# Optimization experiments

Measured on AMD Instinct MI355X. Metric: run time of the kernel, lower is better.

Reference implementation:

```python
import jax, jax.numpy as jnp
import numpy as np
from jax import lax

DN = ('NCDHW', 'OIDHW', 'NCDHW')
ALPHA = 0.1
EPS = 1e-5


def conv3d(x, w, b, padding=1):
    out = lax.conv_general_dilated(x, w, (1, 1, 1), [(padding, padding)] * 3,
                                   dimension_numbers=DN)
    return out + b[None, :, None, None, None]


def conv_transpose3d(x, w, b):
    # PyTorch ConvTranspose3d(k=4, s=2, p=1): equivalent to conv with
    # lhs_dilation=2, flipped kernel, padding k-1-p = 2 per side. Output = 2*D.
    w_c = jnp.flip(jnp.transpose(w, (1, 0, 2, 3, 4)), axis=(2, 3, 4))  # [out,in,4,4,4]
    out = lax.conv_general_dilated(x, w_c, (1, 1, 1), [(2, 2)] * 3,
                                   lhs_dilation=(2, 2, 2), dimension_numbers=DN)
    return out + b[None, :, None, None, None]


def instance_norm(x):
    m = jnp.mean(x, axis=(2, 3, 4), keepdims=True)
    v = jnp.var(x, axis=(2, 3, 4), keepdims=True)
    return (x - m) * lax.rsqrt(v + EPS)


def leaky(x):
    return jnp.where(x >= 0, x, ALPHA * x)


def corr_volume(in1, in2):
    # CorrTorch: 3x3x3 displacement cost volume, mean over channels.
    B, Cc, D, H, W = in1.shape
    in2p = jnp.pad(in2, ((0, 0), (0, 0), (1, 1), (1, 1), (1, 1)))
    vols = []
    for dz in range(3):
        for dy in range(3):
            for dx in range(3):
                win = in2p[:, :, dz:dz + D, dy:dy + H, dx:dx + W]
                vols.append(jnp.mean(in1 * win, axis=1))
    return jnp.stack(vols, axis=1)  # [B, 27, D, H, W]


def setup_inputs() -> dict:
    key = jax.random.key(0)
    ks = jax.random.split(key, 12)
    B, Cf, D = 1, 64, 32  # enc_nf[level-1]=64
    Cin = 3 * 128 + 27    # 411, C channels at level
    Cc = 3 * Cf + 27      # 219
    s = 0.02
    return {
        'src': jax.random.normal(ks[0], (B, Cf, D, D, D), jnp.float32),
        'tgt': jax.random.normal(ks[1], (B, Cf, D, D, D), jnp.float32),
        'C': jax.random.normal(ks[2], (B, Cin, D // 2, D // 2, D // 2), jnp.float32),
        'up_w': jax.random.normal(ks[3], (Cin, Cf, 4, 4, 4), jnp.float32) * s,
        'up_b': jnp.zeros((Cf,), jnp.float32),
        'c1_w': jax.random.normal(ks[4], (Cc, Cc, 3, 3, 3), jnp.float32) * s,
        'c1_b': jnp.zeros((Cc,), jnp.float32),
        'c2_w': jax.random.normal(ks[5], (Cc, Cc, 3, 3, 3), jnp.float32) * s,
        'c2_b': jnp.zeros((Cc,), jnp.float32),
        'out_w': jax.random.normal(ks[6], (3, Cc, 3, 3, 3), jnp.float32) * 1e-5,
        'out_b': jnp.zeros((3,), jnp.float32),
    }


def reference(src, tgt, C, up_w, up_b, c1_w, c1_b, c2_w, c2_b, out_w, out_b):
    Cup = leaky(instance_norm(conv_transpose3d(C, up_w, up_b)))   # upConv
    cost = corr_volume(tgt, src)                                  # CorrTorch(tgt, src)
    x = jnp.concatenate([tgt, src, cost, Cup], axis=1)            # [B,219,D,H,W]
    x = leaky(instance_norm(conv3d(x, c1_w, c1_b)))               # ConvInsBlock 1
    Cn = leaky(instance_norm(conv3d(x, c2_w, c2_b)))              # ConvInsBlock 2
    out = conv3d(Cn, out_w, out_b)                                # flow head
    return (Cn, out)
```

## Files before the change

kernel.cpp:

```cpp
#include <hip/hip_runtime.h>
#include <hip/hip_bf16.h>

#define S3 32768
#define PADD 34
#define PADS (34*34*34)
#define CC 219
#define CF 64
#define CPAD 224
#define CIN_UP 411
#define CUPAD 416
#define ALPHA 0.1f
#define EPS_IN 1e-5f

typedef __attribute__((ext_vector_type(8))) short short8;
typedef __attribute__((ext_vector_type(4))) float floatx4;

__device__ __forceinline__ float lrelu(float v){ return v >= 0.f ? v : ALPHA * v; }
__device__ __forceinline__ unsigned short f2bf(float f){
    unsigned int u = __builtin_bit_cast(unsigned int, f);
    u = (u + 0x7FFFu + ((u >> 16) & 1u)) >> 16;
    return (unsigned short)u;
}
#define LGKM_BARRIER() __asm__ __volatile__("s_waitcnt lgkmcnt(0)\ns_barrier" ::: "memory")

__global__ __launch_bounds__(256) void pad_kernel(const float* __restrict__ src,
                                                  float* __restrict__ dst){
    int idx = blockIdx.x * 256 + threadIdx.x;
    if (idx >= CF * PADS) return;
    int c = idx / PADS, r = idx % PADS;
    int z = r / (PADD*PADD); int r2 = r % (PADD*PADD);
    int y = r2 / PADD, x = r2 % PADD;
    float v = 0.f;
    if (z >= 1 && z <= 32 && y >= 1 && y <= 32 && x >= 1 && x <= 32)
        v = src[((c*32 + (z-1))*32 + (y-1))*32 + (x-1)];
    dst[idx] = v;
}

__global__ __launch_bounds__(256) void corr_kernel(const float* __restrict__ tgt,
                                                   const float* __restrict__ srcp,
                                                   unsigned short* __restrict__ Xp){
    int p = blockIdx.x * 256 + threadIdx.x;
    int z = p >> 10, y = (p >> 5) & 31, x = p & 31;
    float acc[27];
    #pragma unroll
    for (int k = 0; k < 27; k++) acc[k] = 0.f;
    int pbase = ((z+1)*PADD + (y+1))*PADD + (x+1);
    for (int c = 0; c < CF; c++){
        float t = tgt[c*S3 + p];
        const float* sp = srcp + c*PADS + pbase;
        #pragma unroll
        for (int dz = 0; dz < 3; dz++)
            #pragma unroll
            for (int dy = 0; dy < 3; dy++)
                #pragma unroll
                for (int dx = 0; dx < 3; dx++){
                    int k = (dz*3 + dy)*3 + dx;
                    acc[k] += t * sp[(dz-1)*(PADD*PADD) + (dy-1)*PADD + (dx-1)];
                }
    }
    unsigned short cv[27];
    #pragma unroll
    for (int k = 0; k < 27; k++) cv[k] = f2bf(acc[k] * (1.f/64.f));
    size_t bi = ((size_t)(z+1)*1156 + (y+1)*34 + (x+1))*CPAD + 192;
    uint4 o0, o1, o2;
    o0.x = cv[0]  | ((unsigned)cv[1]<<16);  o0.y = cv[2]  | ((unsigned)cv[3]<<16);
    o0.z = cv[4]  | ((unsigned)cv[5]<<16);  o0.w = cv[6]  | ((unsigned)cv[7]<<16);
    o1.x = cv[8]  | ((unsigned)cv[9]<<16);  o1.y = cv[10] | ((unsigned)cv[11]<<16);
    o1.z = cv[12] | ((unsigned)cv[13]<<16); o1.w = cv[14] | ((unsigned)cv[15]<<16);
    o2.x = cv[16] | ((unsigned)cv[17]<<16); o2.y = cv[18] | ((unsigned)cv[19]<<16);
    o2.z = cv[20] | ((unsigned)cv[21]<<16); o2.w = cv[22] | ((unsigned)cv[23]<<16);
    *(uint4*)&Xp[bi]      = o0;
    *(uint4*)&Xp[bi + 8]  = o1;
    *(uint4*)&Xp[bi + 16] = o2;
    *(unsigned int*)&Xp[bi + 24] = cv[24] | ((unsigned)cv[25]<<16);
    Xp[bi + 26] = cv[26];
}

__global__ __launch_bounds__(256) void stats_kernel(const float* __restrict__ xin,
                                                    float* __restrict__ stats, int nch){
    int c = blockIdx.x;
    const float4* p = (const float4*)(xin + (size_t)c * S3);
    float s = 0.f, s2 = 0.f;
    for (int i = threadIdx.x; i < S3/4; i += 256){
        float4 v = p[i];
        s  += v.x + v.y + v.z + v.w;
        s2 += v.x*v.x + v.y*v.y + v.z*v.z + v.w*v.w;
    }
    #pragma unroll
    for (int off = 32; off > 0; off >>= 1){
        s  += __shfl_xor(s,  off);
        s2 += __shfl_xor(s2, off);
    }
    __shared__ float ls[4], ls2[4];
    int wid = threadIdx.x >> 6;
    if ((threadIdx.x & 63) == 0){ ls[wid] = s; ls2[wid] = s2; }
    __syncthreads();
    if (threadIdx.x == 0){
        float S = 0.f, S2 = 0.f;
        #pragma unroll
        for (int w = 0; w < 4; w++){ S += ls[w]; S2 += ls2[w]; }
        float m   = S * (1.f/S3);
        float var = S2 * (1.f/S3) - m*m;
        stats[c]       = m;
        stats[nch + c] = rsqrtf(var + EPS_IN);
    }
}

__global__ __launch_bounds__(256) void norm_apply_kernel(const float* __restrict__ xin,
                                                         const float* __restrict__ stats,
                                                         float* __restrict__ xout, int nch){
    int idx = blockIdx.x * 256 + threadIdx.x;
    int n4  = nch * (S3/4);
    if (idx >= n4) return;
    int c = idx >> 13;
    float m = stats[c], r = stats[nch + c];
    float4 v = ((const float4*)xin)[idx];
    v.x = lrelu((v.x - m) * r);
    v.y = lrelu((v.y - m) * r);
    v.z = lrelu((v.z - m) * r);
    v.w = lrelu((v.w - m) * r);
    ((float4*)xout)[idx] = v;
}

__global__ __launch_bounds__(256) void pack_kernel(const float* __restrict__ src,
        const float* __restrict__ mean, const float* __restrict__ rstd,
        unsigned short* __restrict__ Xp, int Csrc, int dstbase, int donorm){
    __shared__ float sT[64*33];
    const int row = blockIdx.x;
    const int chunk = blockIdx.y;
    const int t = threadIdx.x;
    {
        int c = t >> 2, xq = (t & 3) * 8;
        int csrc = chunk*64 + c;
        float4 v0 = make_float4(0.f,0.f,0.f,0.f), v1 = v0;
        float m = 0.f, r = 1.f;
        if (csrc < Csrc){
            const float4* s4 = (const float4*)&src[(size_t)csrc*S3 + row*32 + xq];
            v0 = s4[0]; v1 = s4[1];
            if (donorm){ m = mean[csrc]; r = rstd[csrc]; }
        }
        if (donorm){
            v0.x = lrelu((v0.x-m)*r); v0.y = lrelu((v0.y-m)*r);
            v0.z = lrelu((v0.z-m)*r); v0.w = lrelu((v0.w-m)*r);
            v1.x = lrelu((v1.x-m)*r); v1.y = lrelu((v1.y-m)*r);
            v1.z = lrelu((v1.z-m)*r); v1.w = lrelu((v1.w-m)*r);
        }
        float* sp = &sT[c*33 + xq];
        sp[0]=v0.x; sp[1]=v0.y; sp[2]=v0.z; sp[3]=v0.w;
        sp[4]=v1.x; sp[5]=v1.y; sp[6]=v1.z; sp[7]=v1.w;
    }
    __syncthreads();
    {
        int x = t >> 3, coff = (t & 7) * 8;
        int dstc = dstbase + chunk*64 + coff;
        if (dstc < CPAD){
            unsigned short u[8];
            #pragma unroll
            for (int j = 0; j < 8; j++) u[j] = f2bf(sT[(coff+j)*33 + x]);
            uint4 o;
            o.x = u[0] | ((unsigned)u[1]<<16);
            o.y = u[2] | ((unsigned)u[3]<<16);
            o.z = u[4] | ((unsigned)u[5]<<16);
            o.w = u[6] | ((unsigned)u[7]<<16);
            int z = row >> 5, y = row & 31;
            size_t pos = (size_t)(z+1)*1156 + (y+1)*34 + (x+1);
            *(uint4*)&Xp[pos*CPAD + dstc] = o;
        }
    }
}

__global__ __launch_bounds__(256) void pack16_kernel(const float* __restrict__ src,
        unsigned short* __restrict__ Cp){
    __shared__ float sT[64*17];
    const int row = blockIdx.x;
    const int chunk = blockIdx.y;
    const int t = threadIdx.x;
    {
        int c = t >> 2, xq = (t & 3) * 4;
        int csrc = chunk*64 + c;
        float4 v = make_float4(0.f,0.f,0.f,0.f);
        if (csrc < CIN_UP)
            v = *(const float4*)&src[(size_t)csrc*4096 + row*16 + xq];
        float* sp = &sT[c*17 + xq];
        sp[0]=v.x; sp[1]=v.y; sp[2]=v.z; sp[3]=v.w;
    }
    __syncthreads();
    {
        int x = t >> 4, coff = (t & 15) * 4;
        int dstc = chunk*64 + coff;
        if (dstc < CUPAD){
            unsigned short u0 = f2bf(sT[(coff+0)*17 + x]);
            unsigned short u1 = f2bf(sT[(coff+1)*17 + x]);
            unsigned short u2 = f2bf(sT[(coff+2)*17 + x]);
            unsigned short u3 = f2bf(sT[(coff+3)*17 + x]);
            uint2 o; o.x = u0 | ((unsigned)u1<<16); o.y = u2 | ((unsigned)u3<<16);
            int z = row >> 4, y = row & 15;
            size_t pos = (size_t)(z+1)*324 + (y+1)*18 + (x+1);
            *(uint2*)&Cp[pos*CUPAD + dstc] = o;
        }
    }
}

__global__ __launch_bounds__(256) void wpack_kernel(const float* __restrict__ w,
        unsigned short* __restrict__ Wt, int perm){
    int idx = blockIdx.x*256 + threadIdx.x;
    int ciin = idx & 31;
    int co   = (idx >> 5) & 255;
    int rest = idx >> 13;
    int cb = rest % 7, tap = rest / 7;
    int ci = cb*32 + ciin;
    float v = 0.f;
    if (co < CC && ci < CC){
        int ciref = ci;
        if (perm) ciref = ci < 128 ? ci : (ci < 192 ? ci + 27 : ci - 64);
        v = w[((size_t)co*CC + ciref)*27 + tap];
    }
    Wt[idx] = f2bf(v);
}

__global__ __launch_bounds__(256) void wpack_out_kernel(const float* __restrict__ w,
        unsigned short* __restrict__ Wt2){
    int idx = blockIdx.x*256 + threadIdx.x;
    if (idx >= 27*7*16*32) return;
    int ciin = idx & 31;
    int co   = (idx >> 5) & 15;
    int rest = idx >> 9;
    int cb = rest % 7, tap = rest / 7;
    int ci = cb*32 + ciin;
    float v = 0.f;
    if (co < 3 && ci < CC)
        v = w[((size_t)co*CC + ci)*27 + tap];
    Wt2[idx] = f2bf(v);
}

__global__ __launch_bounds__(256) void wupack_kernel(const float* __restrict__ w,
        unsigned short* __restrict__ Wu){
    int idx = blockIdx.x*256 + threadIdx.x;
    int ci = idx % CUPAD;
    int rest = idx / CUPAD;
    int co = rest & 63;
    int pj = rest >> 6;
    int j = pj & 7, p = pj >> 3;
    float v = 0.f;
    if (ci < CIN_UP){
        int oz = p>>2, oy = (p>>1)&1, ox = p&1;
        int jz = j>>2, jy = (j>>1)&1, jx = j&1;
        int wz = 3 - oz - 2*jz, wy = 3 - oy - 2*jy, wx = 3 - ox - 2*jx;
        v = w[(((size_t)ci*64 + co)*64) + wz*16 + wy*4 + wx];
    }
    Wu[idx] = f2bf(v);
}

__global__ __launch_bounds__(256,2) void ups_mfma_kernel(const unsigned short* __restrict__ Cp,
        const unsigned short* __restrict__ Wu, float* __restrict__ U){
    __shared__ unsigned short sA[64*40];
    __shared__ unsigned short sB[64*40];
    const int nt = blockIdx.x;
    const int p  = nt >> 6;
    const int zp = (nt >> 2) & 15;
    const int y0 = (nt & 3) * 4;
    const int oz = p>>2, oy = (p>>1)&1, ox = p&1;
    const int t = threadIdx.x, w = t>>6, l = t&63;
    const int mw = (w&1)*32, nw = (w>>1)*32;
    const int lm = l&15, lq = l>>4;
    const int sn = t>>2, spart = (t&3)*8;
    const int sr = sn>>4, sx = sn&15;
    floatx4 acc[2][2];
    #pragma unroll
    for (int i=0;i<2;i++)
        #pragma unroll
        for (int j=0;j<2;j++) acc[i][j] = (floatx4){0.f,0.f,0.f,0.f};

    for (int j = 0; j < 8; ++j){
        int sz = oz + (j>>2), sy = oy + ((j>>1)&1), sxx = ox + (j&1);
        size_t pbase = ((size_t)(zp+sz)*324 + (y0+sr+sy)*18 + (sx+sxx)) * CUPAD;
        size_t abase = ((size_t)(p*8 + j)*64 + sn)*CUPAD;
        for (int cb = 0; cb < 13; ++cb){
            uint4 av = *(const uint4*)&Wu[abase + cb*32 + spart];
            uint4 bv = *(const uint4*)&Cp[pbase + cb*32 + spart];
            *(uint4*)&sA[sn*40 + spart] = av;
            *(uint4*)&sB[sn*40 + spart] = bv;
            __syncthreads();
            short8 af[2], bfv[2];
            #pragma unroll
            for (int i=0;i<2;i++){
                af[i]  = *(const short8*)&sA[(mw + i*16 + lm)*40 + lq*8];
                bfv[i] = *(const short8*)&sB[(nw + i*16 + lm)*40 + lq*8];
            }
            #pragma unroll
            for (int i=0;i<2;i++)
                #pragma unroll
                for (int jj=0;jj<2;jj++)
                    acc[i][jj] = __builtin_amdgcn_mfma_f32_16x16x32_bf16(af[i], bfv[jj], acc[i][jj], 0,0,0);
            __syncthreads();
        }
    }
    #pragma unroll
    for (int i=0;i<2;i++){
        #pragma unroll
        for (int jj=0;jj<2;jj++){
            int n = nw + jj*16 + lm;
            int yy = y0 + (n>>4), xx = n&15;
            size_t opos = ((size_t)(2*zp+oz)<<10) + ((size_t)(2*yy+oy)<<5) + (2*xx+ox);
            #pragma unroll
            for (int r=0;r<4;r++){
                int co = mw + i*16 + lq*4 + r;
                U[(size_t)co*S3 + opos] = acc[i][jj][r];
            }
        }
    }
}

__global__ __launch_bounds__(256,2) void conv_mfma_kernel(const unsigned short* __restrict__ Xp,
        const unsigned short* __restrict__ Wt, const float* __restrict__ bg,
        float* __restrict__ Y){
    __shared__ unsigned short sB[612*40];
    const int nt = blockIdx.x;
    const int mt = blockIdx.y;
    const int z  = nt >> 3;
    const int y0 = (nt & 7) * 4;
    const int t = threadIdx.x, w = t>>6, l = t&63;
    const int mw = (w & 1) * 64, nw = (w >> 1) * 64;
    const int lm = l & 15, lq = l >> 4;
    const unsigned short* ap = Wt + (size_t)(mt*128 + mw + lm)*32 + lq*8;

    floatx4 acc[4][4];
    #pragma unroll
    for (int i=0;i<4;i++)
        #pragma unroll
        for (int j=0;j<4;j++) acc[i][j] = (floatx4){0.f,0.f,0.f,0.f};

    short8 A0[4], A1[4];
    #pragma unroll
    for (int i=0;i<4;i++) A0[i] = *(const short8*)(ap + i*512);
    #pragma unroll
    for (int i=0;i<4;i++) A1[i] = *(const short8*)(ap + (size_t)7*8192 + i*512);

    for (int cb = 0; cb < 7; ++cb){
        LGKM_BARRIER();
        for (int idx = t; idx < 2448; idx += 256){
            int p = idx >> 2, q = idx & 3;
            int zz = p / 204, rem = p % 204;
            int yy = rem / 34, x = rem - yy*34;
            uint4 v = *(const uint4*)&Xp[((size_t)((z+zz)*1156 + (y0+yy)*34 + x))*CPAD + cb*32 + q*8];
            *(uint4*)&sB[p*40 + q*8] = v;
        }
        LGKM_BARRIER();
        #pragma unroll 1
        for (int tap = 0; tap < 27; ++tap){
            int u2 = cb*27 + tap + 2; if (u2 > 188) u2 = 188;
            int cb2 = u2 / 27, tap2 = u2 - cb2*27;
            const unsigned short* apn = ap + (size_t)(tap2*7 + cb2)*8192;
            short8 N0[4];
            #pragma unroll
            for (int i=0;i<4;i++) N0[i] = *(const short8*)(apn + i*512);
            const int dz = tap/9, r9 = tap - dz*9;
            const int dy = r9/3, dx = r9 - dy*3;
            short8 bf[4];
            #pragma unroll
            for (int j=0;j<4;j++){
                int n = nw + j*16 + lm;
                bf[j] = *(const short8*)&sB[(dz*204 + ((n>>5)+dy)*34 + (n&31)+dx)*40 + lq*8];
            }
            #pragma unroll
            for (int i=0;i<4;i++)
                #pragma unroll
                for (int j=0;j<4;j++)
                    acc[i][j] = __builtin_amdgcn_mfma_f32_16x16x32_bf16(A0[i], bf[j], acc[i][j], 0,0,0);
            #pragma unroll
            for (int i=0;i<4;i++){ A0[i] = A1[i]; A1[i] = N0[i]; }
        }
    }
    #pragma unroll
    for (int i=0;i<4;i++){
        #pragma unroll
        for (int j=0;j<4;j++){
            const int n = nw + j*16 + lm;
            const size_t pp = ((size_t)z<<10) + ((size_t)(y0 + (n>>5))<<5) + (n&31);
            #pragma unroll
            for (int r=0;r<4;r++){
                int gm = mt*128 + mw + i*16 + lq*4 + r;
                if (gm < CC) Y[(size_t)gm*S3 + pp] = acc[i][j][r] + bg[gm];
            }
        }
    }
}

__global__ __launch_bounds__(256,2) void convout_mfma_kernel(const unsigned short* __restrict__ Xp,
        const unsigned short* __restrict__ Wt2, const float* __restrict__ bgl,
        float* __restrict__ Y){
    __shared__ unsigned short sB[612*36];
    const int nt = blockIdx.x;
    const int z  = nt >> 3;
    const int y0 = (nt & 7) * 4;
    const int t = threadIdx.x, w = t>>6, l = t&63;
    const int nw = w * 32;
    const int lm = l & 15, lq = l >> 4;
    floatx4 acc[2];
    acc[0] = (floatx4){0.f,0.f,0.f,0.f};
    acc[1] = (floatx4){0.f,0.f,0.f,0.f};

    for (int cb = 0; cb < 7; ++cb){
        __syncthreads();
        for (int idx = t; idx < 2448; idx += 256){
            int p = idx >> 2, q = idx & 3;
            int zz = p / 204, rem = p % 204;
            int yy = rem / 34, x = rem - yy*34;
            uint4 v = *(const uint4*)&Xp[((size_t)((z+zz)*1156 + (y0+yy)*34 + x))*CPAD + cb*32 + q*8];
            *(uint4*)&sB[p*36 + q*8] = v;
        }
        short8 af[27];
        {
            const unsigned short* wp = Wt2 + ((size_t)(cb*16 + lm))*32 + lq*8;
            #pragma unroll
            for (int tap = 0; tap < 27; ++tap)
                af[tap] = *(const short8*)(wp + (size_t)tap*3584);
        }
        __syncthreads();
        #pragma unroll
        for (int tap = 0; tap < 27; ++tap){
            const int dz = tap/9, dy = (tap/3)%3, dx = tap%3;
            #pragma unroll
            for (int j=0;j<2;j++){
                int n = nw + j*16 + lm;
                int r = n >> 5, x = n & 31;
                short8 bf = *(const short8*)&sB[(dz*204 + (r+dy)*34 + (x+dx))*36 + lq*8];
                acc[j] = __builtin_amdgcn_mfma_f32_16x16x32_bf16(af[tap], bf, acc[j], 0,0,0);
            }
        }
    }
    if (lq == 0){
        #pragma unroll
        for (int j = 0; j < 2; j++){
            int n = nw + j*16 + lm;
            size_t pp = ((size_t)z<<10) + ((size_t)(y0 + (n>>5))<<5) + (n&31);
            #pragma unroll
            for (int r = 0; r < 3; r++)
                Y[(size_t)r*S3 + pp] = acc[j][r] + bgl[r];
        }
    }
}

extern "C" void kernel_launch(void* const* d_in, const int* in_sizes, int n_in,
                              void* d_out, int out_size, void* d_ws, size_t ws_size,
                              hipStream_t stream) {
    const float* src   = (const float*)d_in[0];
    const float* tgt   = (const float*)d_in[1];
    const float* Cmat  = (const float*)d_in[2];
    const float* up_w  = (const float*)d_in[3];
    const float* c1_w  = (const float*)d_in[5];
    const float* c1_b  = (const float*)d_in[6];
    const float* c2_w  = (const float*)d_in[7];
    const float* c2_b  = (const float*)d_in[8];
    const float* out_w = (const float*)d_in[9];
    const float* out_b = (const float*)d_in[10];

    float* out = (float*)d_out;
    char* ws = (char*)d_ws;
    unsigned short* Xp = (unsigned short*)ws;
    float*  U  = (float*)(ws + 17608192);
    unsigned short* Wt = (unsigned short*)(ws + 17608192);
    unsigned short* Cp = (unsigned short*)(ws + 25996800);
    unsigned short* Wu = (unsigned short*)(ws + 25996800 + 4852224);
    float* srcp = (float*)(ws + 25996800);
    unsigned short* Wt2 = (unsigned short*)(ws + 25996800);
    float* stats = (float*)(ws + 36058624);

    hipMemsetAsync(Xp, 0, 17608192, stream);
    hipMemsetAsync(Cp, 0, 4852224, stream);

    pack16_kernel<<<dim3(256,7), 256, 0, stream>>>(Cmat, Cp);
    wupack_kernel<<<6656, 256, 0, stream>>>(up_w, Wu);
    ups_mfma_kernel<<<512, 256, 0, stream>>>(Cp, Wu, U);
    stats_kernel<<<64, 256, 0, stream>>>(U, stats, 64);
    pack_kernel<<<dim3(1024,1), 256, 0, stream>>>(U, stats, stats+64, Xp, 64, 128, 1);
    pack_kernel<<<dim3(1024,1), 256, 0, stream>>>(tgt, nullptr, nullptr, Xp, 64, 0, 0);
    pack_kernel<<<dim3(1024,1), 256, 0, stream>>>(src, nullptr, nullptr, Xp, 64, 64, 0);
    pad_kernel<<<9826, 256, 0, stream>>>(src, srcp);
    corr_kernel<<<128, 256, 0, stream>>>(tgt, srcp, Xp);
    wpack_out_kernel<<<378, 256, 0, stream>>>(out_w, Wt2);
    wpack_kernel<<<6048, 256, 0, stream>>>(c1_w, Wt, 1);
    conv_mfma_kernel<<<dim3(256,2), 256, 0, stream>>>(Xp, Wt, c1_b, out);
    stats_kernel<<<219, 256, 0, stream>>>(out, stats, 219);
    pack_kernel<<<dim3(1024,4), 256, 0, stream>>>(out, stats, stats+219, Xp, 219, 0, 1);
    wpack_kernel<<<6048, 256, 0, stream>>>(c2_w, Wt, 0);
    conv_mfma_kernel<<<dim3(256,2), 256, 0, stream>>>(Xp, Wt, c2_b, out);
    stats_kernel<<<219, 256, 0, stream>>>(out, stats, 219);
    pack_kernel<<<dim3(1024,4), 256, 0, stream>>>(out, stats, stats+219, Xp, 219, 0, 1);
    norm_apply_kernel<<<(219*(S3/4))/256, 256, 0, stream>>>(out, stats, out, 219);
    convout_mfma_kernel<<<256, 256, 0, stream>>>(Xp, Wt2, out_b, out + (size_t)CC*S3);
}
```

Baseline: 568.6 us.

## Unroll tap loop, precompute addresses, and stage global loads before barrier

Restructures the main conv MFMA kernel. Shared-memory and global staging offsets are computed once per thread, and all 10 input-tile loads are issued into registers before the barrier so they overlap with the previous block's compute. The 27-tap loop is fully unrolled with a 3-slot register ring for weight prefetch, which removes per-tap integer division and register shuffling. The cost is higher register pressure (vstage, offsets, unrolled body), which could lower occupancy at launch_bounds 2 or cause spills.

```diff
diff --git a/kernel.cpp b/kernel.cpp
--- a/kernel.cpp
+++ b/kernel.cpp
@@ -324,51 +324,71 @@
     const int lm = l & 15, lq = l >> 4;
     const unsigned short* ap = Wt + (size_t)(mt*128 + mw + lm)*32 + lq*8;
 
+    int vB[4];
+    #pragma unroll
+    for (int j=0;j<4;j++){
+        int n = nw + j*16 + lm;
+        vB[j] = ((n>>5)*34 + (n&31))*80 + lq*16;
+    }
+    unsigned int goff[10]; int loff[10];
+    #pragma unroll
+    for (int k=0;k<10;k++){
+        int idx = t + k*256;
+        int p = idx >> 2, q = idx & 3;
+        int zz = p / 204, rem = p % 204;
+        int yy = rem / 34, x = rem - yy*34;
+        goff[k] = (unsigned)((((z+zz)*1156 + (y0+yy)*34 + x)*CPAD + q*8) * 2);
+        loff[k] = (p*40 + q*8) * 2;
+    }
+    const bool full9 = (t < 144);
+
     floatx4 acc[4][4];
     #pragma unroll
     for (int i=0;i<4;i++)
         #pragma unroll
         for (int j=0;j<4;j++) acc[i][j] = (floatx4){0.f,0.f,0.f,0.f};
 
-    short8 A0[4], A1[4];
-    #pragma unroll
-    for (int i=0;i<4;i++) A0[i] = *(const short8*)(ap + i*512);
-    #pragma unroll
-    for (int i=0;i<4;i++) A1[i] = *(const short8*)(ap + (size_t)7*8192 + i*512);
+    short8 Apipe[3][4];
+    #pragma unroll
+    for (int i=0;i<4;i++) Apipe[0][i] = *(const short8*)(ap + i*512);
+    #pragma unroll
+    for (int i=0;i<4;i++) Apipe[1][i] = *(const short8*)(ap + (size_t)57344 + i*512);
 
     for (int cb = 0; cb < 7; ++cb){
+        uint4 vstage[10];
+        {
+            const char* gb = (const char*)Xp + cb*64;
+            #pragma unroll
+            for (int k=0;k<9;k++) vstage[k] = *(const uint4*)(gb + goff[k]);
+            if (full9) vstage[9] = *(const uint4*)(gb + goff[9]);
+        }
         LGKM_BARRIER();
-        for (int idx = t; idx < 2448; idx += 256){
-            int p = idx >> 2, q = idx & 3;
-            int zz = p / 204, rem = p % 204;
-            int yy = rem / 34, x = rem - yy*34;
-            uint4 v = *(const uint4*)&Xp[((size_t)((z+zz)*1156 + (y0+yy)*34 + x))*CPAD + cb*32 + q*8];
-            *(uint4*)&sB[p*40 + q*8] = v;
-        }
+        #pragma unroll
+        for (int k=0;k<9;k++) *(uint4*)((char*)sB + loff[k]) = vstage[k];
+        if (full9) *(uint4*)((char*)sB + loff[9]) = vstage[9];
         LGKM_BARRIER();
-        #pragma unroll 1
+
+        const unsigned short* apc = ap + (size_t)cb*8192;
+        const unsigned short* apn = (cb < 6) ? apc + 8192 : apc;
+        #pragma unroll
         for (int tap = 0; tap < 27; ++tap){
-            int u2 = cb*27 + tap + 2; if (u2 > 188) u2 = 188;
-            int cb2 = u2 / 27, tap2 = u2 - cb2*27;
-            const unsigned short* apn = ap + (size_t)(tap2*7 + cb2)*8192;
-            short8 N0[4];
-            #pragma unroll
-            for (int i=0;i<4;i++) N0[i] = *(const short8*)(apn + i*512);
-            const int dz = tap/9, r9 = tap - dz*9;
-            const int dy = r9/3, dx = r9 - dy*3;
+            const int dz = tap/9, dy = (tap/3)%3, dx = tap%3;
+            const int toff = (dz*204 + dy*34 + dx)*80;
+            {
+                const unsigned short* pn = (tap < 25) ? (apc + (size_t)(tap+2)*57344)
+                                                      : (apn + (size_t)(tap-25)*57344);
+                #pragma unroll
+                for (int i=0;i<4;i++) Apipe[(tap+2)%3][i] = *(const short8*)(pn + i*512);
+            }
             short8 bf[4];
             #pragma unroll
-            for (int j=0;j<4;j++){
-                int n = nw + j*16 + lm;
-                bf[j] = *(const short8*)&sB[(dz*204 + ((n>>5)+dy)*34 + (n&31)+dx)*40 + lq*8];
-            }
+            for (int j=0;j<4;j++)
+                bf[j] = *(const short8*)((const char*)sB + (vB[j] + toff));
             #pragma unroll
             for (int i=0;i<4;i++)
                 #pragma unroll
                 for (int j=0;j<4;j++)
-                    acc[i][j] = __builtin_amdgcn_mfma_f32_16x16x32_bf16(A0[i], bf[j], acc[i][j], 0,0,0);
-            #pragma unroll
-            for (int i=0;i<4;i++){ A0[i] = A1[i]; A1[i] = N0[i]; }
+                    acc[i][j] = __builtin_amdgcn_mfma_f32_16x16x32_bf16(Apipe[tap%3][i], bf[j], acc[i][j], 0,0,0);
         }
     }
     #pragma unroll
```

New measurement: 646.5 us. 1.14x slower.
